# Optimization experiments

Hardware: AMD Instinct MI355X
Metric: run time of the kernel (lower is better)

## Reference

```python
import jax, jax.numpy as jnp
import numpy as np

D = 128      # feature dim
H = 8        # heads
DH = D // H  # dim per head
N = 100000   # nodes
E = 600000   # edges
BN_EPS = 1e-5


def _bn(x, g, b, m, v):
    # BatchNorm1d in eval mode (running stats)
    return (x - m) * jax.lax.rsqrt(v + BN_EPS) * g + b


def setup_inputs() -> dict:
    key = jax.random.key(0)
    ks = jax.random.split(key, 32)
    s = 1.0 / np.sqrt(D)
    inp = {
        "x": jax.random.normal(ks[0], (N, D), jnp.float32),
        "edge_index": jax.random.randint(ks[1], (2, E), 0, N, jnp.int64),
        # type embeddings (1 node type, 1 edge type)
        "nt_emb": jax.random.normal(ks[2], (1, D), jnp.float32),
        "et_emb": jax.random.normal(ks[3], (1, D), jnp.float32),
        # merge_node_edge_attr: Linear(2D,D) -> BN -> ReLU -> Linear(D,D)
        "mW1": jax.random.normal(ks[4], (2 * D, D), jnp.float32) * s,
        "mb1": jnp.zeros((D,), jnp.float32),
        "m_g": jnp.ones((D,), jnp.float32),
        "m_b": jnp.zeros((D,), jnp.float32),
        "m_m": jax.random.normal(ks[5], (D,), jnp.float32) * 0.1,
        "m_v": jax.random.uniform(ks[6], (D,), jnp.float32, 0.5, 1.5),
        "mW2": jax.random.normal(ks[7], (D, D), jnp.float32) * s,
        "mb2": jnp.zeros((D,), jnp.float32),
        # residual projection (no bias)
        "resW": jax.random.normal(ks[8], (D, D), jnp.float32) * s,
        # attention projections
        "qW": jax.random.normal(ks[9], (D, D), jnp.float32) * s,
        "qb": jnp.zeros((D,), jnp.float32),
        "kW": jax.random.normal(ks[10], (D, D), jnp.float32) * s,
        "kb": jnp.zeros((D,), jnp.float32),
        "vW": jax.random.normal(ks[11], (D, D), jnp.float32) * s,
        "vb": jnp.zeros((D,), jnp.float32),
        # output mlp: Linear -> BN -> LeakyReLU -> Linear
        "oW1": jax.random.normal(ks[12], (D, D), jnp.float32) * s,
        "ob1": jnp.zeros((D,), jnp.float32),
        "o_g": jnp.ones((D,), jnp.float32),
        "o_b": jnp.zeros((D,), jnp.float32),
        "o_m": jax.random.normal(ks[13], (D,), jnp.float32) * 0.1,
        "o_v": jax.random.uniform(ks[14], (D,), jnp.float32, 0.5, 1.5),
        "oW2": jax.random.normal(ks[15], (D, D), jnp.float32) * s,
        "ob2": jnp.zeros((D,), jnp.float32),
    }
    return inp


def reference(x, edge_index, nt_emb, et_emb, mW1, mb1, m_g, m_b, m_m, m_v, mW2, mb2,
              resW, qW, qb, kW, kb, vW, vb, oW1, ob1, o_g, o_b, o_m, o_v, oW2, ob2):
    src = edge_index[0]
    dst = edge_index[1]
    n_nodes = x.shape[0]
    e = edge_index.shape[1]

    # GraphNodeEdgeAttr: edge attrs are constant per edge type; with one node
    # type, edge_attr[0] == edge_attr[1] == merge(cat[node_emb, edge_emb]).
    merged = jnp.concatenate([nt_emb[0], et_emb[0]])          # [2D]
    h = jax.nn.relu(_bn(merged @ mW1 + mb1, m_g, m_b, m_m, m_v))
    ea = h @ mW2 + mb2                                        # [D], broadcasts per edge

    # edge_update: per-edge multi-head attention scores
    x_j = x[src]                                              # [E, D] source feats
    x_i = x[dst]                                              # [E, D] target feats
    q = ((x_j + ea) @ qW + qb).reshape(e, H, DH) / jnp.sqrt(jnp.float32(DH))
    k = ((x_i + ea) @ kW + kb).reshape(e, H, DH)
    msg = (x_j @ vW + vb).reshape(e, H, DH)
    scores = jnp.sum(q * k, axis=2)                           # [E, H]

    # segment softmax keyed by source node index
    smax = jax.ops.segment_max(scores, src, num_segments=n_nodes)
    ex = jnp.exp(scores - smax[src])
    ssum = jax.ops.segment_sum(ex, src, num_segments=n_nodes)
    alpha = ex / ssum[src]                                    # [E, H]

    # message + scatter-add aggregation to destination nodes
    weighted = (msg * alpha[:, :, None]).reshape(e, H * DH)   # [E, D]
    aggr = jax.ops.segment_sum(weighted, dst, num_segments=n_nodes)  # [N, D]

    res = x @ resW
    z = aggr + res
    out = jax.nn.leaky_relu(_bn(z @ oW1 + ob1, o_g, o_b, o_m, o_v)) @ oW2 + ob2
    return out
```

## Files before the change

kernel.cpp:

```cpp
#include <hip/hip_runtime.h>

#define BN_EPS 1e-5f
#define SCAN_CHUNK 1024
#define BM 128
#define ZSTRIDE 132

typedef __attribute__((ext_vector_type(8))) short s16x8;
typedef __attribute__((ext_vector_type(4))) float f32x4;

__global__ __launch_bounds__(128) void k_ea(
    const float* __restrict__ nt, const float* __restrict__ et,
    const float* __restrict__ mW1, const float* __restrict__ mb1,
    const float* __restrict__ m_g, const float* __restrict__ m_b,
    const float* __restrict__ m_m, const float* __restrict__ m_v,
    const float* __restrict__ mW2, const float* __restrict__ mb2,
    const float* __restrict__ qW, const float* __restrict__ qb,
    const float* __restrict__ kW, const float* __restrict__ kb,
    float* __restrict__ eaq, float* __restrict__ eak)
{
    __shared__ float merged[256];
    __shared__ float h[128];
    __shared__ float sea[128];
    const int t = threadIdx.x;
    merged[t]       = nt[t];
    merged[128 + t] = et[t];
    __syncthreads();
    float acc = mb1[t];
    for (int i = 0; i < 256; ++i) acc = fmaf(merged[i], mW1[i * 128 + t], acc);
    acc = (acc - m_m[t]) * rsqrtf(m_v[t] + BN_EPS) * m_g[t] + m_b[t];
    h[t] = acc > 0.f ? acc : 0.f;
    __syncthreads();
    float acc2 = mb2[t];
    for (int k = 0; k < 128; ++k) acc2 = fmaf(h[k], mW2[k * 128 + t], acc2);
    sea[t] = acc2;
    __syncthreads();
    float aq = qb[t], ak = kb[t];
    for (int k = 0; k < 128; ++k) {
        const float e = sea[k];
        aq = fmaf(e, qW[k * 128 + t], aq);
        ak = fmaf(e, kW[k * 128 + t], ak);
    }
    eaq[t] = aq;
    eak[t] = ak;
}

__device__ __forceinline__ void split_store(float w, ushort* __restrict__ base,
                                            int j, int k)
{
    unsigned u = __builtin_bit_cast(unsigned, w);
    unsigned hi = (u + 0x7fffu + ((u >> 16) & 1u)) >> 16;
    float hif = __builtin_bit_cast(float, hi << 16);
    float res = w - hif;
    unsigned lo = __builtin_bit_cast(unsigned, res) >> 16;
    base[j * 128 + k]         = (ushort)hi;
    base[16384 + j * 128 + k] = (ushort)lo;
}

__global__ __launch_bounds__(128) void k_prep3(
    const float* __restrict__ W0, const float* __restrict__ W1,
    const float* __restrict__ W2, ushort* __restrict__ P)
{
    const int j = blockIdx.x;
    const int m = blockIdx.y;
    const int k = threadIdx.x;
    const float* W = (m == 0) ? W0 : (m == 1) ? W1 : W2;
    split_store(W[k * 128 + j], P + (size_t)m * 32768, j, k);
}

__global__ __launch_bounds__(128) void k_prep_out(
    const float* __restrict__ resW, const float* __restrict__ oW1,
    const float* __restrict__ oW2, ushort* __restrict__ P)
{
    __shared__ float col[128];
    const int j = blockIdx.x;
    const int m = blockIdx.y;
    const int k = threadIdx.x;
    float w;
    if (m == 0) {
        col[k] = oW1[k * 128 + j];
        __syncthreads();
        float acc = 0.f;
        for (int i = 0; i < 128; ++i) acc = fmaf(resW[k * 128 + i], col[i], acc);
        w = acc;
    } else {
        const float* W = (m == 1) ? oW1 : oW2;
        w = W[k * 128 + j];
    }
    split_store(w, P + (size_t)m * 32768, j, k);
}

template <int NT>
__device__ __forceinline__ void stage_w(const ushort* __restrict__ wpl,
                                        ushort* __restrict__ sw, int tid)
{
    const uint4* src = (const uint4*)wpl;
#pragma unroll
    for (int it = 0; it < 4096 / NT; ++it) {
        const int idx = it * NT + tid;
        const uint4 v = src[idx];
        const int plane = idx >> 11;
        const int rr = (idx >> 4) & 127;
        const int cb = (idx & 15) << 4;
        const int byteoff = ((rr * 256 + cb) ^ ((rr & 7) << 4));
        *(uint4*)((char*)sw + plane * 32768 + byteoff) = v;
    }
}

template <int CT>
__device__ __forceinline__ void mm_core(const float* __restrict__ Arow,
                                        const ushort* __restrict__ sw,
                                        int g, int r16, int ct0, f32x4* acc)
{
#pragma unroll
    for (int ks = 0; ks < 4; ++ks) {
        const float* ap = Arow + ks * 32 + g * 8;
        const float4 a0 = *(const float4*)(ap);
        const float4 a1 = *(const float4*)(ap + 4);
        float av[8] = {a0.x, a0.y, a0.z, a0.w, a1.x, a1.y, a1.z, a1.w};
        s16x8 ahi, alo;
#pragma unroll
        for (int j = 0; j < 8; ++j) {
            const unsigned u = __builtin_bit_cast(unsigned, av[j]);
            ahi[j] = (short)(u >> 16);
            const float hif = __builtin_bit_cast(float, u & 0xffff0000u);
            const float res = av[j] - hif;
            alo[j] = (short)(__builtin_bit_cast(unsigned, res) >> 16);
        }
        const int koff = ks * 64 + g * 16;
#pragma unroll
        for (int ct = 0; ct < CT; ++ct) {
            const int row = (ct0 + ct) * 16 + r16;
            const int byteoff = ((row * 256 + koff) ^ ((row & 7) << 4));
            const s16x8 bhi = *(const s16x8*)((const char*)sw + byteoff);
            const s16x8 blo = *(const s16x8*)((const char*)sw + 32768 + byteoff);
            acc[ct] = __builtin_amdgcn_mfma_f32_16x16x32_bf16(ahi, bhi, acc[ct], 0, 0, 0);
            acc[ct] = __builtin_amdgcn_mfma_f32_16x16x32_bf16(ahi, blo, acc[ct], 0, 0, 0);
            acc[ct] = __builtin_amdgcn_mfma_f32_16x16x32_bf16(alo, bhi, acc[ct], 0, 0, 0);
        }
    }
}

__global__ __launch_bounds__(512, 4) void k_mm_qkv(
    const float* __restrict__ x, const ushort* __restrict__ planes,
    const float* __restrict__ eaq, const float* __restrict__ eak,
    const float* __restrict__ vb,
    float* __restrict__ Q, float* __restrict__ K, float* __restrict__ V, int N)
{
    __shared__ ushort sw[2 * 128 * 128];
    const int tid = threadIdx.x;
    const int sel = blockIdx.y;
    stage_w<512>(planes + (size_t)sel * 32768, sw, tid);
    __syncthreads();

    const int wave = tid >> 6, lane = tid & 63;
    const int g = lane >> 4, r16 = lane & 15;
    const int n0 = blockIdx.x * BM + wave * 16;
    int nA = n0 + r16; if (nA >= N) nA = N - 1;

    f32x4 acc[8];
#pragma unroll
    for (int ct = 0; ct < 8; ++ct) acc[ct] = (f32x4){0.f, 0.f, 0.f, 0.f};
    mm_core<8>(x + (size_t)nA * 128, sw, g, r16, 0, acc);

    const float* bias = (sel == 0) ? eaq : (sel == 1) ? eak : vb;
    float* O          = (sel == 0) ? Q   : (sel == 1) ? K   : V;
    const float scale = (sel == 0) ? 0.25f : 1.0f;
#pragma unroll
    for (int ct = 0; ct < 8; ++ct) {
        const int c = ct * 16 + r16;
        const float bc = bias[c];
#pragma unroll
        for (int r = 0; r < 4; ++r) {
            const int n = n0 + g * 4 + r;
            if (n < N) O[(size_t)n * 128 + c] = (acc[ct][r] + bc) * scale;
        }
    }
}

__global__ __launch_bounds__(1024, 4) void k_out2(
    const float* __restrict__ x, const ushort* __restrict__ Po,
    const float* __restrict__ aggr,
    const float* __restrict__ ob1,
    const float* __restrict__ o_m, const float* __restrict__ o_v,
    const float* __restrict__ o_g, const float* __restrict__ o_b,
    const float* __restrict__ ob2,
    float* __restrict__ out, int N)
{
    __shared__ ushort sw[2 * 128 * 128];
    __shared__ float  tb[128 * ZSTRIDE];
    const int tid = threadIdx.x;
    const int wave = tid >> 6, lane = tid & 63;
    const int g = lane >> 4, r16 = lane & 15;
    const int wr = wave & 7, wc = wave >> 3;
    const int ct0 = wc * 4;
    const int n0 = blockIdx.x * BM;
    const int arow = wr * 16 + r16;
    int nA = n0 + arow; if (nA >= N) nA = N - 1;

    f32x4 acc[4];
#pragma unroll
    for (int ct = 0; ct < 4; ++ct) acc[ct] = (f32x4){0.f, 0.f, 0.f, 0.f};

    stage_w<1024>(Po, sw, tid);
    __syncthreads();
    mm_core<4>(x + (size_t)nA * 128, sw, g, r16, ct0, acc);
    __syncthreads();

    stage_w<1024>(Po + 32768, sw, tid);
    __syncthreads();
    mm_core<4>(aggr + (size_t)nA * 128, sw, g, r16, ct0, acc);
    __syncthreads();

#pragma unroll
    for (int ct = 0; ct < 4; ++ct) {
        const int c = (ct0 + ct) * 16 + r16;
        const float bc = ob1[c];
        const float rs = rsqrtf(o_v[c] + BN_EPS);
        const float mm = o_m[c], gg = o_g[c], bb = o_b[c];
#pragma unroll
        for (int r = 0; r < 4; ++r) {
            const int nrel = wr * 16 + g * 4 + r;
            float u = acc[ct][r] + bc;
            u = (u - mm) * rs * gg + bb;
            u = u > 0.f ? u : 0.01f * u;
            tb[nrel * ZSTRIDE + c] = u;
        }
    }
    stage_w<1024>(Po + 65536, sw, tid);
    __syncthreads();

#pragma unroll
    for (int ct = 0; ct < 4; ++ct) acc[ct] = (f32x4){0.f, 0.f, 0.f, 0.f};
    mm_core<4>(tb + arow * ZSTRIDE, sw, g, r16, ct0, acc);
#pragma unroll
    for (int ct = 0; ct < 4; ++ct) {
        const int c = (ct0 + ct) * 16 + r16;
        const float bc = ob2[c];
#pragma unroll
        for (int r = 0; r < 4; ++r) {
            const int n = n0 + wr * 16 + g * 4 + r;
            if (n < N) out[(size_t)n * 128 + c] = acc[ct][r] + bc;
        }
    }
}

__global__ __launch_bounds__(256) void k_edge1csr(
    const int* __restrict__ esrc, const int* __restrict__ row_start,
    const int* __restrict__ deg, const float* __restrict__ Q,
    const float* __restrict__ K, float* __restrict__ exp_,
    float* __restrict__ ssum, int N)
{
    const int tid = threadIdx.x;
    const int n = blockIdx.x * 4 + (tid >> 6);
    if (n >= N) return;
    const int lane = tid & 63;
    const int sub = lane >> 5;
    const int l = lane & 31;
    const int h = l >> 2;
    const int c0 = l * 4;
    const int rs = row_start[n];
    const int dg = deg[n];
    const float4 kreg = *(const float4*)(K + (size_t)n * 128 + c0);
    for (int j = sub; j < dg; j += 2) {
        const int idx = rs + j;
        const int s = esrc[idx];
        const float4 q = *(const float4*)(Q + (size_t)s * 128 + c0);
        float p = q.x * kreg.x + q.y * kreg.y + q.z * kreg.z + q.w * kreg.w;
        p += __shfl_xor(p, 1, 64);
        p += __shfl_xor(p, 2, 64);
        if ((l & 3) == 0) {
            const float v = __expf(p);
            exp_[(size_t)idx * 8 + h] = v;
            unsafeAtomicAdd(&ssum[(size_t)s * 8 + h], v);
        }
    }
}

__global__ __launch_bounds__(256) void k_vscale(
    float* __restrict__ V, const float* __restrict__ ssum, int N)
{
    const int i = blockIdx.x * 256 + threadIdx.x;
    if (i >= N * 32) return;
    const int row = i >> 5, q = i & 31, h = q >> 2;
    const float r = 1.0f / ssum[(size_t)row * 8 + h];
    float4 v = *(float4*)(V + (size_t)i * 4);
    v.x *= r; v.y *= r; v.z *= r; v.w *= r;
    *(float4*)(V + (size_t)i * 4) = v;
}

__global__ __launch_bounds__(256) void k_hist(const int* __restrict__ ei,
                                              int* __restrict__ deg, int E)
{
    const int e = blockIdx.x * 256 + threadIdx.x;
    if (e < E) atomicAdd(&deg[ei[E + e]], 1);
}

__global__ __launch_bounds__(256) void k_scan_partial(const int* __restrict__ deg,
                                                      int* __restrict__ part, int N)
{
    __shared__ int sd[256];
    const int b = blockIdx.x, t = threadIdx.x;
    const int base = b * SCAN_CHUNK + t * 4;
    int s = 0;
#pragma unroll
    for (int i = 0; i < 4; ++i) { const int idx = base + i; if (idx < N) s += deg[idx]; }
    sd[t] = s; __syncthreads();
    for (int off = 128; off > 0; off >>= 1) {
        if (t < off) sd[t] += sd[t + off];
        __syncthreads();
    }
    if (t == 0) part[b] = sd[0];
}

__global__ __launch_bounds__(256) void k_scan_top(int* __restrict__ part, int nb)
{
    __shared__ int sd[256];
    const int t = threadIdx.x;
    const int orig = (t < nb) ? part[t] : 0;
    sd[t] = orig;
    __syncthreads();
    for (int off = 1; off < 256; off <<= 1) {
        const int v = (t >= off) ? sd[t - off] : 0;
        __syncthreads();
        sd[t] += v;
        __syncthreads();
    }
    if (t < nb) part[t] = sd[t] - orig;
}

__global__ __launch_bounds__(256) void k_scan_final(const int* __restrict__ deg,
                                                    const int* __restrict__ part,
                                                    int* __restrict__ row_start,
                                                    int* __restrict__ cursor, int N)
{
    __shared__ int ts[256];
    const int b = blockIdx.x, t = threadIdx.x;
    const int base = b * SCAN_CHUNK + t * 4;
    int v[4]; int s = 0;
#pragma unroll
    for (int i = 0; i < 4; ++i) { const int idx = base + i; v[i] = (idx < N) ? deg[idx] : 0; s += v[i]; }
    ts[t] = s; __syncthreads();
    for (int off = 1; off < 256; off <<= 1) {
        const int vv = (t >= off) ? ts[t - off] : 0;
        __syncthreads();
        ts[t] += vv;
        __syncthreads();
    }
    int run = part[b] + ((t > 0) ? ts[t - 1] : 0);
#pragma unroll
    for (int i = 0; i < 4; ++i) {
        const int idx = base + i;
        if (idx < N) { row_start[idx] = run; cursor[idx] = run; run += v[i]; }
    }
}

__global__ __launch_bounds__(256) void k_scatter(const int* __restrict__ ei,
                                                 int* __restrict__ cursor,
                                                 int* __restrict__ esrc, int E)
{
    const int e = blockIdx.x * 256 + threadIdx.x;
    if (e < E) {
        const int pos = atomicAdd(&cursor[ei[E + e]], 1);
        esrc[pos] = ei[e];
    }
}

__global__ __launch_bounds__(256) void k_aggr(
    const int* __restrict__ esrc, const int* __restrict__ row_start,
    const int* __restrict__ deg, const float* __restrict__ V,
    const float* __restrict__ exp_, float* __restrict__ aggr, int N)
{
    const int tid = threadIdx.x;
    const int n = blockIdx.x * 4 + (tid >> 6);
    if (n >= N) return;
    const int lane = tid & 63;
    const int sub = lane >> 5;
    const int l = lane & 31;
    const int h = l >> 2;
    const int c0 = l * 4;
    const int rs = row_start[n];
    const int dg = deg[n];
    float4 acc = make_float4(0.f, 0.f, 0.f, 0.f);
    for (int j = sub; j < dg; j += 2) {
        const int idx = rs + j;
        const int s = esrc[idx];
        const float a = exp_[(size_t)idx * 8 + h];
        const float4 v = *(const float4*)(V + (size_t)s * 128 + c0);
        acc.x = fmaf(v.x, a, acc.x);
        acc.y = fmaf(v.y, a, acc.y);
        acc.z = fmaf(v.z, a, acc.z);
        acc.w = fmaf(v.w, a, acc.w);
    }
    acc.x += __shfl_xor(acc.x, 32, 64);
    acc.y += __shfl_xor(acc.y, 32, 64);
    acc.z += __shfl_xor(acc.z, 32, 64);
    acc.w += __shfl_xor(acc.w, 32, 64);
    if (sub == 0) *(float4*)(aggr + (size_t)n * 128 + c0) = acc;
}

extern "C" void kernel_launch(void* const* d_in, const int* in_sizes, int n_in,
                              void* d_out, int out_size, void* d_ws, size_t ws_size,
                              hipStream_t stream)
{
    const float* x    = (const float*)d_in[0];
    const int*   ei   = (const int*)d_in[1];
    const float* nt   = (const float*)d_in[2];
    const float* et   = (const float*)d_in[3];
    const float* mW1  = (const float*)d_in[4];
    const float* mb1  = (const float*)d_in[5];
    const float* m_g  = (const float*)d_in[6];
    const float* m_b  = (const float*)d_in[7];
    const float* m_m  = (const float*)d_in[8];
    const float* m_v  = (const float*)d_in[9];
    const float* mW2  = (const float*)d_in[10];
    const float* mb2  = (const float*)d_in[11];
    const float* resW = (const float*)d_in[12];
    const float* qW   = (const float*)d_in[13];
    const float* qb   = (const float*)d_in[14];
    const float* kW   = (const float*)d_in[15];
    const float* kb   = (const float*)d_in[16];
    const float* vW   = (const float*)d_in[17];
    const float* vb   = (const float*)d_in[18];
    const float* oW1  = (const float*)d_in[19];
    const float* ob1  = (const float*)d_in[20];
    const float* o_g  = (const float*)d_in[21];
    const float* o_b  = (const float*)d_in[22];
    const float* o_m  = (const float*)d_in[23];
    const float* o_v  = (const float*)d_in[24];
    const float* oW2  = (const float*)d_in[25];
    const float* ob2  = (const float*)d_in[26];
    float* out = (float*)d_out;

    const int N = in_sizes[0] / 128;
    const int E = in_sizes[1] / 2;

    float* ws   = (float*)d_ws;
    float* eaq  = ws;
    float* eak  = ws + 128;
    float* Q    = ws + 256;
    float* K    = Q + (size_t)N * 128;
    float* V    = K + (size_t)N * 128;
    float* exp_ = V + (size_t)N * 128;
    float* ssum = exp_ + (size_t)E * 8;
    int* deg       = (int*)(ssum + (size_t)N * 8);
    int* row_start = deg + N;
    int* cursor    = row_start + N;
    int* part      = cursor + N;
    int* esrc      = part + 256;
    float* aggr = Q;
    ushort* Pq = (ushort*)ssum;
    ushort* Po = (ushort*)exp_;

    const int nbm  = (N + BM - 1) / BM;
    const int nbsc = (N + SCAN_CHUNK - 1) / SCAN_CHUNK;

    k_prep3<<<dim3(128, 3), 128, 0, stream>>>(qW, kW, vW, Pq);
    k_ea<<<1, 128, 0, stream>>>(nt, et, mW1, mb1, m_g, m_b, m_m, m_v, mW2, mb2,
                                qW, qb, kW, kb, eaq, eak);
    k_mm_qkv<<<dim3(nbm, 3), 512, 0, stream>>>(x, Pq, eaq, eak, vb, Q, K, V, N);

    hipMemsetAsync(ssum, 0, (size_t)N * 8 * sizeof(float), stream);
    hipMemsetAsync(deg, 0, (size_t)N * sizeof(int), stream);

    k_hist<<<(E + 255) / 256, 256, 0, stream>>>(ei, deg, E);
    k_scan_partial<<<nbsc, 256, 0, stream>>>(deg, part, N);
    k_scan_top<<<1, 256, 0, stream>>>(part, nbsc);
    k_scan_final<<<nbsc, 256, 0, stream>>>(deg, part, row_start, cursor, N);
    k_scatter<<<(E + 255) / 256, 256, 0, stream>>>(ei, cursor, esrc, E);

    k_edge1csr<<<(N + 3) / 4, 256, 0, stream>>>(esrc, row_start, deg, Q, K, exp_, ssum, N);
    k_vscale<<<(N * 32 + 255) / 256, 256, 0, stream>>>(V, ssum, N);
    k_aggr<<<(N + 3) / 4, 256, 0, stream>>>(esrc, row_start, deg, V, exp_, aggr, N);

    k_prep_out<<<dim3(128, 3), 128, 0, stream>>>(resW, oW1, oW2, Po);
    k_out2<<<nbm, 1024, 0, stream>>>(x, Po, aggr, ob1, o_m, o_v, o_g, o_b, ob2, out, N);
}
```

Baseline: 496.9 us.

## Store V in bf16, scale exp weights per edge, split output MLP into two kernels

V is now written in bf16, which halves the bytes of the random gathers in the aggregation kernel. The per-node V rescale is replaced by a reciprocal pass on ssum followed by a per-edge scaling of the exp weights. The QKV matmul moves to 1024-thread blocks with a 2D wave tiling. The fused output kernel is split in two: the first writes the hidden activation as bf16 hi/lo planes to global memory, and the second runs the final matmul. This removes the large LDS buffer, at the cost of extra global traffic and precision loss in V.

```diff
diff --git a/kernel.cpp b/kernel.cpp
--- a/kernel.cpp
+++ b/kernel.cpp
@@ -3,10 +3,20 @@
 #define BN_EPS 1e-5f
 #define SCAN_CHUNK 1024
 #define BM 128
-#define ZSTRIDE 132
 
 typedef __attribute__((ext_vector_type(8))) short s16x8;
 typedef __attribute__((ext_vector_type(4))) float f32x4;
+
+__device__ __forceinline__ ushort f2bf_rne(float f)
+{
+    unsigned u = __builtin_bit_cast(unsigned, f);
+    return (ushort)((u + 0x7fffu + ((u >> 16) & 1u)) >> 16);
+}
+
+__device__ __forceinline__ float bf2f(ushort u)
+{
+    return __builtin_bit_cast(float, (unsigned)u << 16);
+}
 
 __global__ __launch_bounds__(128) void k_ea(
     const float* __restrict__ nt, const float* __restrict__ et,
@@ -140,54 +150,91 @@
     }
 }
 
-__global__ __launch_bounds__(512, 4) void k_mm_qkv(
+template <int CT>
+__device__ __forceinline__ void mm_core_pre(const ushort* __restrict__ Ahi,
+                                            const ushort* __restrict__ Alo,
+                                            const ushort* __restrict__ sw,
+                                            int g, int r16, int ct0, f32x4* acc)
+{
+#pragma unroll
+    for (int ks = 0; ks < 4; ++ks) {
+        const s16x8 ahi = *(const s16x8*)(Ahi + ks * 32 + g * 8);
+        const s16x8 alo = *(const s16x8*)(Alo + ks * 32 + g * 8);
+        const int koff = ks * 64 + g * 16;
+#pragma unroll
+        for (int ct = 0; ct < CT; ++ct) {
+            const int row = (ct0 + ct) * 16 + r16;
+            const int byteoff = ((row * 256 + koff) ^ ((row & 7) << 4));
+            const s16x8 bhi = *(const s16x8*)((const char*)sw + byteoff);
+            const s16x8 blo = *(const s16x8*)((const char*)sw + 32768 + byteoff);
+            acc[ct] = __builtin_amdgcn_mfma_f32_16x16x32_bf16(ahi, bhi, acc[ct], 0, 0, 0);
+            acc[ct] = __builtin_amdgcn_mfma_f32_16x16x32_bf16(ahi, blo, acc[ct], 0, 0, 0);
+            acc[ct] = __builtin_amdgcn_mfma_f32_16x16x32_bf16(alo, bhi, acc[ct], 0, 0, 0);
+        }
+    }
+}
+
+__global__ __launch_bounds__(1024, 8) void k_mm_qkv(
     const float* __restrict__ x, const ushort* __restrict__ planes,
     const float* __restrict__ eaq, const float* __restrict__ eak,
     const float* __restrict__ vb,
-    float* __restrict__ Q, float* __restrict__ K, float* __restrict__ V, int N)
+    float* __restrict__ Q, float* __restrict__ K, ushort* __restrict__ V16, int N)
 {
     __shared__ ushort sw[2 * 128 * 128];
     const int tid = threadIdx.x;
     const int sel = blockIdx.y;
-    stage_w<512>(planes + (size_t)sel * 32768, sw, tid);
+    stage_w<1024>(planes + (size_t)sel * 32768, sw, tid);
     __syncthreads();
 
     const int wave = tid >> 6, lane = tid & 63;
     const int g = lane >> 4, r16 = lane & 15;
-    const int n0 = blockIdx.x * BM + wave * 16;
-    int nA = n0 + r16; if (nA >= N) nA = N - 1;
-
-    f32x4 acc[8];
-#pragma unroll
-    for (int ct = 0; ct < 8; ++ct) acc[ct] = (f32x4){0.f, 0.f, 0.f, 0.f};
-    mm_core<8>(x + (size_t)nA * 128, sw, g, r16, 0, acc);
-
-    const float* bias = (sel == 0) ? eaq : (sel == 1) ? eak : vb;
-    float* O          = (sel == 0) ? Q   : (sel == 1) ? K   : V;
-    const float scale = (sel == 0) ? 0.25f : 1.0f;
-#pragma unroll
-    for (int ct = 0; ct < 8; ++ct) {
-        const int c = ct * 16 + r16;
-        const float bc = bias[c];
-#pragma unroll
-        for (int r = 0; r < 4; ++r) {
-            const int n = n0 + g * 4 + r;
-            if (n < N) O[(size_t)n * 128 + c] = (acc[ct][r] + bc) * scale;
-        }
-    }
-}
-
-__global__ __launch_bounds__(1024, 4) void k_out2(
+    const int wr = wave & 7, wc = wave >> 3;
+    const int ct0 = wc * 4;
+    const int n0 = blockIdx.x * BM;
+    const int arow = wr * 16 + r16;
+    int nA = n0 + arow; if (nA >= N) nA = N - 1;
+
+    f32x4 acc[4];
+#pragma unroll
+    for (int ct = 0; ct < 4; ++ct) acc[ct] = (f32x4){0.f, 0.f, 0.f, 0.f};
+    mm_core<4>(x + (size_t)nA * 128, sw, g, r16, ct0, acc);
+
+    if (sel == 2) {
+#pragma unroll
+        for (int ct = 0; ct < 4; ++ct) {
+            const int c = (ct0 + ct) * 16 + r16;
+            const float bc = vb[c];
+#pragma unroll
+            for (int r = 0; r < 4; ++r) {
+                const int n = n0 + wr * 16 + g * 4 + r;
+                if (n < N) V16[(size_t)n * 128 + c] = f2bf_rne(acc[ct][r] + bc);
+            }
+        }
+    } else {
+        const float* bias = sel ? eak : eaq;
+        float* O          = sel ? K   : Q;
+        const float scale = sel ? 1.0f : 0.25f;
+#pragma unroll
+        for (int ct = 0; ct < 4; ++ct) {
+            const int c = (ct0 + ct) * 16 + r16;
+            const float bc = bias[c];
+#pragma unroll
+            for (int r = 0; r < 4; ++r) {
+                const int n = n0 + wr * 16 + g * 4 + r;
+                if (n < N) O[(size_t)n * 128 + c] = (acc[ct][r] + bc) * scale;
+            }
+        }
+    }
+}
+
+__global__ __launch_bounds__(1024, 8) void k_out_u(
     const float* __restrict__ x, const ushort* __restrict__ Po,
-    const float* __restrict__ aggr,
-    const float* __restrict__ ob1,
+    const float* __restrict__ aggr, const float* __restrict__ ob1,
     const float* __restrict__ o_m, const float* __restrict__ o_v,
     const float* __restrict__ o_g, const float* __restrict__ o_b,
-    const float* __restrict__ ob2,
-    float* __restrict__ out, int N)
+    ushort* __restrict__ t_hi, ushort* __restrict__ t_lo, int N)
 {
     __shared__ ushort sw[2 * 128 * 128];
-    __shared__ float  tb[128 * ZSTRIDE];
     const int tid = threadIdx.x;
     const int wave = tid >> 6, lane = tid & 63;
     const int g = lane >> 4, r16 = lane & 15;
@@ -205,11 +252,9 @@
     __syncthreads();
     mm_core<4>(x + (size_t)nA * 128, sw, g, r16, ct0, acc);
     __syncthreads();
-
     stage_w<1024>(Po + 32768, sw, tid);
     __syncthreads();
     mm_core<4>(aggr + (size_t)nA * 128, sw, g, r16, ct0, acc);
-    __syncthreads();
 
 #pragma unroll
     for (int ct = 0; ct < 4; ++ct) {
@@ -219,19 +264,44 @@
         const float mm = o_m[c], gg = o_g[c], bb = o_b[c];
 #pragma unroll
         for (int r = 0; r < 4; ++r) {
-            const int nrel = wr * 16 + g * 4 + r;
+            const int n = n0 + wr * 16 + g * 4 + r;
+            if (n >= N) continue;
             float u = acc[ct][r] + bc;
             u = (u - mm) * rs * gg + bb;
             u = u > 0.f ? u : 0.01f * u;
-            tb[nrel * ZSTRIDE + c] = u;
-        }
-    }
-    stage_w<1024>(Po + 65536, sw, tid);
-    __syncthreads();
-
+            const unsigned uu = __builtin_bit_cast(unsigned, u);
+            const unsigned hi = (uu + 0x7fffu + ((uu >> 16) & 1u)) >> 16;
+            const float hif = __builtin_bit_cast(float, hi << 16);
+            const unsigned lo = __builtin_bit_cast(unsigned, u - hif) >> 16;
+            t_hi[(size_t)n * 128 + c] = (ushort)hi;
+            t_lo[(size_t)n * 128 + c] = (ushort)lo;
+        }
+    }
+}
+
+__global__ __launch_bounds__(1024, 8) void k_out_f(
+    const ushort* __restrict__ t_hi, const ushort* __restrict__ t_lo,
+    const ushort* __restrict__ Pw, const float* __restrict__ ob2,
+    float* __restrict__ out, int N)
+{
+    __shared__ ushort sw[2 * 128 * 128];
+    const int tid = threadIdx.x;
+    stage_w<1024>(Pw, sw, tid);
+    __syncthreads();
+
+    const int wave = tid >> 6, lane = tid & 63;
+    const int g = lane >> 4, r16 = lane & 15;
+    const int wr = wave & 7, wc = wave >> 3;
+    const int ct0 = wc * 4;
+    const int n0 = blockIdx.x * BM;
+    const int arow = wr * 16 + r16;
+    int nA = n0 + arow; if (nA >= N) nA = N - 1;
+
+    f32x4 acc[4];
 #pragma unroll
     for (int ct = 0; ct < 4; ++ct) acc[ct] = (f32x4){0.f, 0.f, 0.f, 0.f};
-    mm_core<4>(tb + arow * ZSTRIDE, sw, g, r16, ct0, acc);
+    mm_core_pre<4>(t_hi + (size_t)nA * 128, t_lo + (size_t)nA * 128, sw, g, r16, ct0, acc);
+
 #pragma unroll
     for (int ct = 0; ct < 4; ++ct) {
         const int c = (ct0 + ct) * 16 + r16;
@@ -276,16 +346,19 @@
     }
 }
 
-__global__ __launch_bounds__(256) void k_vscale(
-    float* __restrict__ V, const float* __restrict__ ssum, int N)
+__global__ __launch_bounds__(256) void k_rsum(float* __restrict__ ssum, int M)
 {
     const int i = blockIdx.x * 256 + threadIdx.x;
-    if (i >= N * 32) return;
-    const int row = i >> 5, q = i & 31, h = q >> 2;
-    const float r = 1.0f / ssum[(size_t)row * 8 + h];
-    float4 v = *(float4*)(V + (size_t)i * 4);
-    v.x *= r; v.y *= r; v.z *= r; v.w *= r;
-    *(float4*)(V + (size_t)i * 4) = v;
+    if (i < M) ssum[i] = 1.0f / ssum[i];
+}
+
+__global__ __launch_bounds__(256) void k_escale(
+    float* __restrict__ exp_, const int* __restrict__ esrc,
+    const float* __restrict__ rsum, int EH)
+{
+    const int i = blockIdx.x * 256 + threadIdx.x;
+    if (i >= EH) return;
+    exp_[i] *= rsum[(size_t)esrc[i >> 3] * 8 + (i & 7)];
 }
 
 __global__ __launch_bounds__(256) void k_hist(const int* __restrict__ ei,
@@ -367,7 +440,7 @@
 
 __global__ __launch_bounds__(256) void k_aggr(
     const int* __restrict__ esrc, const int* __restrict__ row_start,
-    const int* __restrict__ deg, const float* __restrict__ V,
+    const int* __restrict__ deg, const ushort* __restrict__ V16,
     const float* __restrict__ exp_, float* __restrict__ aggr, int N)
 {
     const int tid = threadIdx.x;
@@ -385,11 +458,11 @@
         const int idx = rs + j;
         const int s = esrc[idx];
         const float a = exp_[(size_t)idx * 8 + h];
-        const float4 v = *(const float4*)(V + (size_t)s * 128 + c0);
-        acc.x = fmaf(v.x, a, acc.x);
-        acc.y = fmaf(v.y, a, acc.y);
-        acc.z = fmaf(v.z, a, acc.z);
-        acc.w = fmaf(v.w, a, acc.w);
+        const ushort4 vu = *(const ushort4*)(V16 + (size_t)s * 128 + c0);
+        acc.x = fmaf(bf2f(vu.x), a, acc.x);
+        acc.y = fmaf(bf2f(vu.y), a, acc.y);
+        acc.z = fmaf(bf2f(vu.z), a, acc.z);
+        acc.w = fmaf(bf2f(vu.w), a, acc.w);
     }
     acc.x += __shfl_xor(acc.x, 32, 64);
     acc.y += __shfl_xor(acc.y, 32, 64);
@@ -448,6 +521,9 @@
     int* part      = cursor + N;
     int* esrc      = part + 256;
     float* aggr = Q;
+    ushort* V16 = (ushort*)V;
+    ushort* t_hi = (ushort*)K;
+    ushort* t_lo = t_hi + (size_t)N * 128;
     ushort* Pq = (ushort*)ssum;
     ushort* Po = (ushort*)exp_;
 
@@ -457,7 +533,7 @@
     k_prep3<<<dim3(128, 3), 128, 0, stream>>>(qW, kW, vW, Pq);
     k_ea<<<1, 128, 0, stream>>>(nt, et, mW1, mb1, m_g, m_b, m_m, m_v, mW2, mb2,
                                 qW, qb, kW, kb, eaq, eak);
-    k_mm_qkv<<<dim3(nbm, 3), 512, 0, stream>>>(x, Pq, eaq, eak, vb, Q, K, V, N);
+    k_mm_qkv<<<dim3(nbm, 3), 1024, 0, stream>>>(x, Pq, eaq, eak, vb, Q, K, V16, N);
 
     hipMemsetAsync(ssum, 0, (size_t)N * 8 * sizeof(float), stream);
     hipMemsetAsync(deg, 0, (size_t)N * sizeof(int), stream);
@@ -469,9 +545,11 @@
     k_scatter<<<(E + 255) / 256, 256, 0, stream>>>(ei, cursor, esrc, E);
 
     k_edge1csr<<<(N + 3) / 4, 256, 0, stream>>>(esrc, row_start, deg, Q, K, exp_, ssum, N);
-    k_vscale<<<(N * 32 + 255) / 256, 256, 0, stream>>>(V, ssum, N);
-    k_aggr<<<(N + 3) / 4, 256, 0, stream>>>(esrc, row_start, deg, V, exp_, aggr, N);
+    k_rsum<<<(N * 8 + 255) / 256, 256, 0, stream>>>(ssum, N * 8);
+    k_escale<<<(E * 8 + 255) / 256, 256, 0, stream>>>(exp_, esrc, ssum, E * 8);
+    k_aggr<<<(N + 3) / 4, 256, 0, stream>>>(esrc, row_start, deg, V16, exp_, aggr, N);
 
     k_prep_out<<<dim3(128, 3), 128, 0, stream>>>(resW, oW1, oW2, Po);
-    k_out2<<<nbm, 1024, 0, stream>>>(x, Po, aggr, ob1, o_m, o_v, o_g, o_b, ob2, out, N);
-}
+    k_out_u<<<nbm, 1024, 0, stream>>>(x, Po, aggr, ob1, o_m, o_v, o_g, o_b, t_hi, t_lo, N);
+    k_out_f<<<nbm, 1024, 0, stream>>>(t_hi, t_lo, Po + 65536, ob2, out, N);
+}
```

New measurement: 521.2 us. 4.9% more time.
